# Optimization experiments

Measured on AMD Instinct MI355X. Metric: run time of the kernel, lower is better.

Reference implementation:

```python
import jax, jax.numpy as jnp
import numpy as np

B, NA, DIN, H, DOUT = 8192, 32, 8, 64, 8  # B must be divisible by NA (final reshape)


def setup_inputs() -> dict:
    key = jax.random.key(0)
    ks = jax.random.split(key, 9)
    rn = lambda k, shp, s=1.0: jax.random.normal(k, shp, dtype=jnp.float32) * s
    return {
        "x": rn(ks[0], (B, NA, DIN)),
        "laplacian": jax.random.uniform(ks[1], (B, NA, 1), dtype=jnp.float32),
        "W_in": rn(ks[2], (H, DIN), 1.0 / np.sqrt(DIN)),
        "b_in": rn(ks[3], (H,), 0.01),
        "Aq": rn(ks[4], (H, H)),   # torch.randn init in original
        "Ak": rn(ks[5], (H, H)),
        "Av": rn(ks[6], (H, H)),
        "W_out": rn(ks[7], (DOUT, H), 1.0 / np.sqrt(H)),
        "b_out": rn(ks[8], (DOUT,), 0.01),
    }


def reference(x, laplacian, W_in, b_in, Aq, Ak, Av, W_out, b_out):
    silu = jax.nn.silu
    # mlp_in = SiLU(Linear); kron(laplacian, ones(1,1,H)) == broadcast of (B,na,1) mask
    h = silu(x @ W_in.T + b_in) * laplacian            # (B, na, H)
    # Q/K/V: weight @ h^T with swish; attention is over the HIDDEN axis (H x H scores)
    Q = silu(jnp.einsum('ij,bnj->bin', Aq, h))         # (B, H, na)
    K = silu(jnp.einsum('ij,bnj->bni', Ak, h))         # (B, na, H)
    V = silu(jnp.einsum('ij,bnj->bin', Av, h))         # (B, H, na)
    A = jax.nn.softmax(jnp.einsum('bin,bnj->bij', Q, K), axis=2)  # (B, H, H), softmax dim=2
    attn = silu(jnp.einsum('bij,bjn->bni', A, V))      # (B, na, H)
    # mlp_out = SiLU(Linear), masked again, mean over nodes, reshape (B/na, na, O)
    y = silu(attn @ W_out.T + b_out) * laplacian       # (B, na, O)
    return y.mean(axis=1).reshape(-1, NA, DOUT)        # (B/NA, NA, O)
```

## Files before the change

kernel.cpp:

```cpp
#include <hip/hip_runtime.h>

#define NB   8192
#define NA   32
#define DIN  8
#define HID  64
#define DOUT 8

typedef float     v4f __attribute__((ext_vector_type(4)));
typedef __fp16    v2fp __attribute__((ext_vector_type(2)));
typedef _Float16  v2h __attribute__((ext_vector_type(2)));
typedef _Float16  v4h __attribute__((ext_vector_type(4)));
typedef _Float16  v8h __attribute__((ext_vector_type(8)));

__device__ __forceinline__ float silu_f(float x) {
    return __fdividef(x, 1.0f + __expf(-x));
}

__device__ __forceinline__ v2h pkrtz(float a, float b) {
    v2fp r = __builtin_amdgcn_cvt_pkrtz(a, b);
    return __builtin_bit_cast(v2h, r);
}

__device__ __forceinline__ v4h cvt4(v4f a) {
    v2h lo = pkrtz(a[0], a[1]);
    v2h hi = pkrtz(a[2], a[3]);
    return __builtin_shufflevector(lo, hi, 0, 1, 2, 3);
}

__device__ __forceinline__ v8h cvt8(v4f a, v4f b) {
    v4h x = cvt4(a);
    v4h y = cvt4(b);
    return __builtin_shufflevector(x, y, 0, 1, 2, 3, 4, 5, 6, 7);
}

__device__ __forceinline__ v4h silu_cvt4(v4f a) {
    v4f s;
    s[0] = silu_f(a[0]); s[1] = silu_f(a[1]);
    s[2] = silu_f(a[2]); s[3] = silu_f(a[3]);
    return cvt4(s);
}

__device__ __forceinline__ v8h cat(v4h a, v4h b) {
    return __builtin_shufflevector(a, b, 0, 1, 2, 3, 4, 5, 6, 7);
}

#define MFMA16(A, B, C) __builtin_amdgcn_mfma_f32_16x16x16f16((A), (B), (C), 0, 0, 0)
#define MFMA32(A, B, C) __builtin_amdgcn_mfma_f32_16x16x32_f16((A), (B), (C), 0, 0, 0)
#define STAGE_FENCE()   __builtin_amdgcn_sched_barrier(0)

__global__ __launch_bounds__(512, 4) void attn_mfma_kernel(
    const float* __restrict__ x,
    const float* __restrict__ lap,
    const float* __restrict__ W_in,
    const float* __restrict__ b_in,
    const float* __restrict__ Aq,
    const float* __restrict__ Ak,
    const float* __restrict__ Av,
    const float* __restrict__ W_out,
    const float* __restrict__ b_out,
    float* __restrict__ out)
{
    __shared__ _Float16 wlds[3][8][64][8];

    const int t  = threadIdx.x;
    const int l  = t & 63;
    const int w  = t >> 6;
    const int lm = l & 15;
    const int lg = l >> 4;

    {
        const float* mats[3] = {Aq, Ak, Av};
        const int it = w >> 1, c = w & 1;
        #pragma unroll
        for (int m = 0; m < 3; ++m) {
            const float* base = mats[m] + (lm + 16 * it) * 64 + 32 * c + 4 * lg;
            v4f va = *(const v4f*)(base);
            v4f vb = *(const v4f*)(base + 16);
            *(v8h*)&wlds[m][w][l][0] = cvt8(va, vb);
        }
    }

    v4h zh = {};
    v4f zf = {};
    v4h winf[4];
    #pragma unroll
    for (int jt = 0; jt < 4; ++jt) {
        v4h wf = zh;
        if (lg < 2)       wf = cvt4(*(const v4f*)(W_in + (lm + 16 * jt) * 8 + 4 * lg));
        else if (lg == 2) wf[0] = (_Float16)b_in[lm + 16 * jt];
        winf[jt] = wf;
    }
    v4h woutf[4];
    #pragma unroll
    for (int ks = 0; ks < 4; ++ks)
        woutf[ks] = (lm < 8) ? cvt4(*(const v4f*)(W_out + lm * 64 + 16 * ks + 4 * lg)) : zh;
    const float boutf = (lm < 8) ? b_out[lm] : 0.0f;
    v4h onef = zh;
    if (lg == 2) onef[0] = (_Float16)1.0f;

    __syncthreads();

    const int b = blockIdx.x * 8 + w;

    v4f lapv[2];
    lapv[0] = *(const v4f*)(lap + b * 32 + 4 * lg);
    lapv[1] = *(const v4f*)(lap + b * 32 + 16 + 4 * lg);
    float lap_n[2];
    lap_n[0] = lap[b * 32 + lm];
    lap_n[1] = lap[b * 32 + 16 + lm];

    v4h xf[2];
    #pragma unroll
    for (int nt = 0; nt < 2; ++nt)
        xf[nt] = (lg < 2) ? cvt4(*(const v4f*)(x + b * 256 + (lm + 16 * nt) * 8 + 4 * lg))
                          : onef;

    v8h hf8[2][2];
    #pragma unroll
    for (int nt = 0; nt < 2; ++nt)
        #pragma unroll
        for (int c = 0; c < 2; ++c) {
            v4h lo, hi;
            {
                v4f hc = MFMA16(winf[2 * c], xf[nt], zf);
                v4f s;
                #pragma unroll
                for (int r = 0; r < 4; ++r) s[r] = silu_f(hc[r]) * lap_n[nt];
                lo = cvt4(s);
            }
            {
                v4f hc = MFMA16(winf[2 * c + 1], xf[nt], zf);
                v4f s;
                #pragma unroll
                for (int r = 0; r < 4; ++r) s[r] = silu_f(hc[r]) * lap_n[nt];
                hi = cvt4(s);
            }
            hf8[nt][c] = cat(lo, hi);
        }
    STAGE_FENCE();

    v8h qf8[4];
    {
        v4f acc[2][4] = {};
        #pragma unroll
        for (int it = 0; it < 4; ++it)
            #pragma unroll
            for (int c = 0; c < 2; ++c) {
                v8h bw = *(v8h*)&wlds[0][it * 2 + c][l][0];
                #pragma unroll
                for (int nt = 0; nt < 2; ++nt)
                    acc[nt][it] = MFMA32(hf8[nt][c], bw, acc[nt][it]);
            }
        #pragma unroll
        for (int it = 0; it < 4; ++it)
            qf8[it] = cat(silu_cvt4(acc[0][it]), silu_cvt4(acc[1][it]));
    }
    STAGE_FENCE();

    v8h kf8[4];
    {
        v4f acc[2][4] = {};
        #pragma unroll
        for (int it = 0; it < 4; ++it)
            #pragma unroll
            for (int c = 0; c < 2; ++c) {
                v8h bw = *(v8h*)&wlds[1][it * 2 + c][l][0];
                #pragma unroll
                for (int nt = 0; nt < 2; ++nt)
                    acc[nt][it] = MFMA32(hf8[nt][c], bw, acc[nt][it]);
            }
        #pragma unroll
        for (int it = 0; it < 4; ++it)
            kf8[it] = cat(silu_cvt4(acc[0][it]), silu_cvt4(acc[1][it]));
    }
    STAGE_FENCE();

    v8h vf8[2][2];
    {
        v4f acc[4][2] = {};
        #pragma unroll
        for (int it = 0; it < 4; ++it)
            #pragma unroll
            for (int c = 0; c < 2; ++c) {
                v8h aw = *(v8h*)&wlds[2][it * 2 + c][l][0];
                #pragma unroll
                for (int nt = 0; nt < 2; ++nt)
                    acc[it][nt] = MFMA32(aw, hf8[nt][c], acc[it][nt]);
            }
        #pragma unroll
        for (int c = 0; c < 2; ++c)
            #pragma unroll
            for (int nt = 0; nt < 2; ++nt)
                vf8[c][nt] = cat(silu_cvt4(acc[2 * c][nt]), silu_cvt4(acc[2 * c + 1][nt]));
    }
    STAGE_FENCE();

    v4f ya[2] = {};
    #pragma unroll
    for (int it = 0; it < 4; ++it) {
        v4f s[4];
        #pragma unroll
        for (int jt = 0; jt < 4; ++jt)
            s[jt] = MFMA32(kf8[jt], qf8[it], zf);

        float mx = fmaxf(fmaxf(fmaxf(s[0][0], s[0][1]), fmaxf(s[0][2], s[0][3])),
                         fmaxf(fmaxf(s[1][0], s[1][1]), fmaxf(s[1][2], s[1][3])));
        float mx2 = fmaxf(fmaxf(fmaxf(s[2][0], s[2][1]), fmaxf(s[2][2], s[2][3])),
                          fmaxf(fmaxf(s[3][0], s[3][1]), fmaxf(s[3][2], s[3][3])));
        mx = fmaxf(mx, mx2);
        mx = fmaxf(mx, __shfl_xor(mx, 16, 64));
        mx = fmaxf(mx, __shfl_xor(mx, 32, 64));
        float sum = 0.0f;
        #pragma unroll
        for (int jt = 0; jt < 4; ++jt)
            #pragma unroll
            for (int r = 0; r < 4; ++r) {
                float e = __expf(s[jt][r] - mx);
                s[jt][r] = e;
                sum += e;
            }
        sum += __shfl_xor(sum, 16, 64);
        sum += __shfl_xor(sum, 32, 64);
        const float inv = __fdividef(1.0f, sum);
        v4h pf[4];
        #pragma unroll
        for (int jt = 0; jt < 4; ++jt) pf[jt] = cvt4(s[jt] * inv);

        v4f pv[2] = {};
        #pragma unroll
        for (int c = 0; c < 2; ++c) {
            v8h pf8 = cat(pf[2 * c], pf[2 * c + 1]);
            #pragma unroll
            for (int nt = 0; nt < 2; ++nt)
                pv[nt] = MFMA32(pf8, vf8[c][nt], pv[nt]);
        }

        #pragma unroll
        for (int nt = 0; nt < 2; ++nt)
            ya[nt] = MFMA16(silu_cvt4(pv[nt]), woutf[it], ya[nt]);
    }

    float acc = 0.0f;
    #pragma unroll
    for (int nt = 0; nt < 2; ++nt)
        #pragma unroll
        for (int r = 0; r < 4; ++r)
            acc += silu_f(ya[nt][r] + boutf) * lapv[nt][r];
    acc += __shfl_xor(acc, 16, 64);
    acc += __shfl_xor(acc, 32, 64);
    if (l < 8) out[b * DOUT + l] = acc * (1.0f / NA);
}

extern "C" void kernel_launch(void* const* d_in, const int* in_sizes, int n_in,
                              void* d_out, int out_size, void* d_ws, size_t ws_size,
                              hipStream_t stream) {
    const float* x     = (const float*)d_in[0];
    const float* lap   = (const float*)d_in[1];
    const float* W_in  = (const float*)d_in[2];
    const float* b_in  = (const float*)d_in[3];
    const float* Aq    = (const float*)d_in[4];
    const float* Ak    = (const float*)d_in[5];
    const float* Av    = (const float*)d_in[6];
    const float* W_out = (const float*)d_in[7];
    const float* b_out = (const float*)d_in[8];
    attn_mfma_kernel<<<1024, 512, 0, stream>>>(x, lap, W_in, b_in, Aq, Ak, Av,
                                               W_out, b_out, (float*)d_out);
}
```

Baseline: 58.79 us.

## Process two batch items per wavefront with 256-thread blocks

Each wavefront now handles two batch elements instead of one, so the block shrinks to 4 waves (256 threads) while still covering 8 items per block. Each LDS weight fragment is loaded once and reused across both items, and the two independent items give the scheduler more MFMA work to interleave. The sched_barrier stage fences are removed so the compiler can reorder freely. In exchange, register pressure roughly doubles per wave, which may lower occupancy or cause spills, and launch bounds move to (256,2).

```diff
diff --git a/kernel.cpp b/kernel.cpp
--- a/kernel.cpp
+++ b/kernel.cpp
@@ -44,11 +44,19 @@
     return __builtin_shufflevector(a, b, 0, 1, 2, 3, 4, 5, 6, 7);
 }
 
+__device__ __forceinline__ float redmax64(float x) {
+    x = fmaxf(x, __shfl_xor(x, 16, 64));
+    return fmaxf(x, __shfl_xor(x, 32, 64));
+}
+__device__ __forceinline__ float redsum64(float x) {
+    x += __shfl_xor(x, 16, 64);
+    return x + __shfl_xor(x, 32, 64);
+}
+
 #define MFMA16(A, B, C) __builtin_amdgcn_mfma_f32_16x16x16f16((A), (B), (C), 0, 0, 0)
 #define MFMA32(A, B, C) __builtin_amdgcn_mfma_f32_16x16x32_f16((A), (B), (C), 0, 0, 0)
-#define STAGE_FENCE()   __builtin_amdgcn_sched_barrier(0)
-
-__global__ __launch_bounds__(512, 4) void attn_mfma_kernel(
+
+__global__ __launch_bounds__(256, 2) void attn_mfma_kernel(
     const float* __restrict__ x,
     const float* __restrict__ lap,
     const float* __restrict__ W_in,
@@ -70,14 +78,15 @@
 
     {
         const float* mats[3] = {Aq, Ak, Av};
-        const int it = w >> 1, c = w & 1;
-        #pragma unroll
-        for (int m = 0; m < 3; ++m) {
-            const float* base = mats[m] + (lm + 16 * it) * 64 + 32 * c + 4 * lg;
-            v4f va = *(const v4f*)(base);
-            v4f vb = *(const v4f*)(base + 16);
-            *(v8h*)&wlds[m][w][l][0] = cvt8(va, vb);
-        }
+        #pragma unroll
+        for (int m = 0; m < 3; ++m)
+            #pragma unroll
+            for (int f = 0; f < 2; ++f) {
+                const int fid = w * 2 + f;
+                const float* base = mats[m] + (lm + 16 * w) * 64 + 32 * f + 4 * lg;
+                *(v8h*)&wlds[m][fid][l][0] =
+                    cvt8(*(const v4f*)base, *(const v4f*)(base + 16));
+            }
     }
 
     v4h zh = {};
@@ -100,155 +109,155 @@
 
     __syncthreads();
 
-    const int b = blockIdx.x * 8 + w;
-
-    v4f lapv[2];
-    lapv[0] = *(const v4f*)(lap + b * 32 + 4 * lg);
-    lapv[1] = *(const v4f*)(lap + b * 32 + 16 + 4 * lg);
-    float lap_n[2];
-    lap_n[0] = lap[b * 32 + lm];
-    lap_n[1] = lap[b * 32 + 16 + lm];
-
-    v4h xf[2];
-    #pragma unroll
-    for (int nt = 0; nt < 2; ++nt)
-        xf[nt] = (lg < 2) ? cvt4(*(const v4f*)(x + b * 256 + (lm + 16 * nt) * 8 + 4 * lg))
-                          : onef;
-
-    v8h hf8[2][2];
-    #pragma unroll
-    for (int nt = 0; nt < 2; ++nt)
+    const int b0 = blockIdx.x * 8 + w * 2;
+
+    v4f  lapv[2][2];
+    float lap_n[2][2];
+    v4h  xf_[2][2];
+    #pragma unroll
+    for (int u = 0; u < 2; ++u) {
+        const int b = b0 + u;
+        lapv[u][0] = *(const v4f*)(lap + b * 32 + 4 * lg);
+        lapv[u][1] = *(const v4f*)(lap + b * 32 + 16 + 4 * lg);
+        lap_n[u][0] = lap[b * 32 + lm];
+        lap_n[u][1] = lap[b * 32 + 16 + lm];
+        #pragma unroll
+        for (int nt = 0; nt < 2; ++nt)
+            xf_[u][nt] = (lg < 2)
+                ? cvt4(*(const v4f*)(x + b * 256 + (lm + 16 * nt) * 8 + 4 * lg))
+                : onef;
+    }
+
+    v8h hf8[2][2][2];
+    #pragma unroll
+    for (int u = 0; u < 2; ++u)
+        #pragma unroll
+        for (int nt = 0; nt < 2; ++nt)
+            #pragma unroll
+            for (int c = 0; c < 2; ++c) {
+                v4f h0 = MFMA16(winf[2 * c],     xf_[u][nt], zf);
+                v4f h1 = MFMA16(winf[2 * c + 1], xf_[u][nt], zf);
+                v4f s0, s1;
+                #pragma unroll
+                for (int r = 0; r < 4; ++r) {
+                    s0[r] = silu_f(h0[r]) * lap_n[u][nt];
+                    s1[r] = silu_f(h1[r]) * lap_n[u][nt];
+                }
+                hf8[u][nt][c] = cat(cvt4(s0), cvt4(s1));
+            }
+
+    v8h qf8[2][4];
+    #pragma unroll
+    for (int it = 0; it < 4; ++it) {
+        v4f a_[2][2] = {};
         #pragma unroll
         for (int c = 0; c < 2; ++c) {
-            v4h lo, hi;
-            {
-                v4f hc = MFMA16(winf[2 * c], xf[nt], zf);
-                v4f s;
-                #pragma unroll
-                for (int r = 0; r < 4; ++r) s[r] = silu_f(hc[r]) * lap_n[nt];
-                lo = cvt4(s);
-            }
-            {
-                v4f hc = MFMA16(winf[2 * c + 1], xf[nt], zf);
-                v4f s;
-                #pragma unroll
-                for (int r = 0; r < 4; ++r) s[r] = silu_f(hc[r]) * lap_n[nt];
-                hi = cvt4(s);
-            }
-            hf8[nt][c] = cat(lo, hi);
-        }
-    STAGE_FENCE();
-
-    v8h qf8[4];
-    {
-        v4f acc[2][4] = {};
-        #pragma unroll
-        for (int it = 0; it < 4; ++it)
-            #pragma unroll
-            for (int c = 0; c < 2; ++c) {
-                v8h bw = *(v8h*)&wlds[0][it * 2 + c][l][0];
+            v8h bw = *(v8h*)&wlds[0][it * 2 + c][l][0];
+            #pragma unroll
+            for (int u = 0; u < 2; ++u)
                 #pragma unroll
                 for (int nt = 0; nt < 2; ++nt)
-                    acc[nt][it] = MFMA32(hf8[nt][c], bw, acc[nt][it]);
-            }
-        #pragma unroll
-        for (int it = 0; it < 4; ++it)
-            qf8[it] = cat(silu_cvt4(acc[0][it]), silu_cvt4(acc[1][it]));
-    }
-    STAGE_FENCE();
-
-    v8h kf8[4];
-    {
-        v4f acc[2][4] = {};
-        #pragma unroll
-        for (int it = 0; it < 4; ++it)
-            #pragma unroll
-            for (int c = 0; c < 2; ++c) {
-                v8h bw = *(v8h*)&wlds[1][it * 2 + c][l][0];
+                    a_[u][nt] = MFMA32(hf8[u][nt][c], bw, a_[u][nt]);
+        }
+        #pragma unroll
+        for (int u = 0; u < 2; ++u)
+            qf8[u][it] = cat(silu_cvt4(a_[u][0]), silu_cvt4(a_[u][1]));
+    }
+    v8h kf8[2][4];
+    #pragma unroll
+    for (int it = 0; it < 4; ++it) {
+        v4f a_[2][2] = {};
+        #pragma unroll
+        for (int c = 0; c < 2; ++c) {
+            v8h bw = *(v8h*)&wlds[1][it * 2 + c][l][0];
+            #pragma unroll
+            for (int u = 0; u < 2; ++u)
                 #pragma unroll
                 for (int nt = 0; nt < 2; ++nt)
-                    acc[nt][it] = MFMA32(hf8[nt][c], bw, acc[nt][it]);
-            }
-        #pragma unroll
-        for (int it = 0; it < 4; ++it)
-            kf8[it] = cat(silu_cvt4(acc[0][it]), silu_cvt4(acc[1][it]));
-    }
-    STAGE_FENCE();
-
-    v8h vf8[2][2];
-    {
-        v4f acc[4][2] = {};
-        #pragma unroll
-        for (int it = 0; it < 4; ++it)
+                    a_[u][nt] = MFMA32(hf8[u][nt][c], bw, a_[u][nt]);
+        }
+        #pragma unroll
+        for (int u = 0; u < 2; ++u)
+            kf8[u][it] = cat(silu_cvt4(a_[u][0]), silu_cvt4(a_[u][1]));
+    }
+    v8h vf8[2][2][2];
+    #pragma unroll
+    for (int cp = 0; cp < 2; ++cp) {
+        v4f a_[2][2][2] = {};
+        #pragma unroll
+        for (int its = 0; its < 2; ++its) {
+            const int it = cp * 2 + its;
             #pragma unroll
             for (int c = 0; c < 2; ++c) {
                 v8h aw = *(v8h*)&wlds[2][it * 2 + c][l][0];
                 #pragma unroll
+                for (int u = 0; u < 2; ++u)
+                    #pragma unroll
+                    for (int nt = 0; nt < 2; ++nt)
+                        a_[its][u][nt] = MFMA32(aw, hf8[u][nt][c], a_[its][u][nt]);
+            }
+        }
+        #pragma unroll
+        for (int u = 0; u < 2; ++u)
+            #pragma unroll
+            for (int nt = 0; nt < 2; ++nt)
+                vf8[u][cp][nt] = cat(silu_cvt4(a_[0][u][nt]), silu_cvt4(a_[1][u][nt]));
+    }
+
+    v4f ya[2][2] = {};
+    #pragma unroll
+    for (int it = 0; it < 4; ++it)
+        #pragma unroll
+        for (int u = 0; u < 2; ++u) {
+            v4f s[4];
+            #pragma unroll
+            for (int jt = 0; jt < 4; ++jt)
+                s[jt] = MFMA32(kf8[u][jt], qf8[u][it], zf);
+
+            float mx = fmaxf(fmaxf(fmaxf(s[0][0], s[0][1]), fmaxf(s[0][2], s[0][3])),
+                             fmaxf(fmaxf(s[1][0], s[1][1]), fmaxf(s[1][2], s[1][3])));
+            float mx2 = fmaxf(fmaxf(fmaxf(s[2][0], s[2][1]), fmaxf(s[2][2], s[2][3])),
+                              fmaxf(fmaxf(s[3][0], s[3][1]), fmaxf(s[3][2], s[3][3])));
+            mx = redmax64(fmaxf(mx, mx2));
+            float sum = 0.0f;
+            #pragma unroll
+            for (int jt = 0; jt < 4; ++jt)
+                #pragma unroll
+                for (int r = 0; r < 4; ++r) {
+                    float e = __expf(s[jt][r] - mx);
+                    s[jt][r] = e;
+                    sum += e;
+                }
+            sum = redsum64(sum);
+            const float inv = __fdividef(1.0f, sum);
+            v4h pf[4];
+            #pragma unroll
+            for (int jt = 0; jt < 4; ++jt) pf[jt] = cvt4(s[jt] * inv);
+
+            v4f pv[2] = {};
+            #pragma unroll
+            for (int c = 0; c < 2; ++c) {
+                v8h pf8 = cat(pf[2 * c], pf[2 * c + 1]);
+                #pragma unroll
                 for (int nt = 0; nt < 2; ++nt)
-                    acc[it][nt] = MFMA32(aw, hf8[nt][c], acc[it][nt]);
-            }
-        #pragma unroll
-        for (int c = 0; c < 2; ++c)
+                    pv[nt] = MFMA32(pf8, vf8[u][c][nt], pv[nt]);
+            }
             #pragma unroll
             for (int nt = 0; nt < 2; ++nt)
-                vf8[c][nt] = cat(silu_cvt4(acc[2 * c][nt]), silu_cvt4(acc[2 * c + 1][nt]));
-    }
-    STAGE_FENCE();
-
-    v4f ya[2] = {};
-    #pragma unroll
-    for (int it = 0; it < 4; ++it) {
-        v4f s[4];
-        #pragma unroll
-        for (int jt = 0; jt < 4; ++jt)
-            s[jt] = MFMA32(kf8[jt], qf8[it], zf);
-
-        float mx = fmaxf(fmaxf(fmaxf(s[0][0], s[0][1]), fmaxf(s[0][2], s[0][3])),
-                         fmaxf(fmaxf(s[1][0], s[1][1]), fmaxf(s[1][2], s[1][3])));
-        float mx2 = fmaxf(fmaxf(fmaxf(s[2][0], s[2][1]), fmaxf(s[2][2], s[2][3])),
-                          fmaxf(fmaxf(s[3][0], s[3][1]), fmaxf(s[3][2], s[3][3])));
-        mx = fmaxf(mx, mx2);
-        mx = fmaxf(mx, __shfl_xor(mx, 16, 64));
-        mx = fmaxf(mx, __shfl_xor(mx, 32, 64));
-        float sum = 0.0f;
-        #pragma unroll
-        for (int jt = 0; jt < 4; ++jt)
-            #pragma unroll
-            for (int r = 0; r < 4; ++r) {
-                float e = __expf(s[jt][r] - mx);
-                s[jt][r] = e;
-                sum += e;
-            }
-        sum += __shfl_xor(sum, 16, 64);
-        sum += __shfl_xor(sum, 32, 64);
-        const float inv = __fdividef(1.0f, sum);
-        v4h pf[4];
-        #pragma unroll
-        for (int jt = 0; jt < 4; ++jt) pf[jt] = cvt4(s[jt] * inv);
-
-        v4f pv[2] = {};
-        #pragma unroll
-        for (int c = 0; c < 2; ++c) {
-            v8h pf8 = cat(pf[2 * c], pf[2 * c + 1]);
-            #pragma unroll
-            for (int nt = 0; nt < 2; ++nt)
-                pv[nt] = MFMA32(pf8, vf8[c][nt], pv[nt]);
-        }
-
+                ya[u][nt] = MFMA16(silu_cvt4(pv[nt]), woutf[it], ya[u][nt]);
+        }
+
+    #pragma unroll
+    for (int u = 0; u < 2; ++u) {
+        float acc = 0.0f;
         #pragma unroll
         for (int nt = 0; nt < 2; ++nt)
-            ya[nt] = MFMA16(silu_cvt4(pv[nt]), woutf[it], ya[nt]);
-    }
-
-    float acc = 0.0f;
-    #pragma unroll
-    for (int nt = 0; nt < 2; ++nt)
-        #pragma unroll
-        for (int r = 0; r < 4; ++r)
-            acc += silu_f(ya[nt][r] + boutf) * lapv[nt][r];
-    acc += __shfl_xor(acc, 16, 64);
-    acc += __shfl_xor(acc, 32, 64);
-    if (l < 8) out[b * DOUT + l] = acc * (1.0f / NA);
+            #pragma unroll
+            for (int r = 0; r < 4; ++r)
+                acc += silu_f(ya[u][nt][r] + boutf) * lapv[u][nt][r];
+        acc = redsum64(acc);
+        if (l < 8) out[(b0 + u) * DOUT + l] = acc * (1.0f / NA);
+    }
 }
 
 extern "C" void kernel_launch(void* const* d_in, const int* in_sizes, int n_in,
@@ -263,6 +272,6 @@
     const float* Av    = (const float*)d_in[6];
     const float* W_out = (const float*)d_in[7];
     const float* b_out = (const float*)d_in[8];
-    attn_mfma_kernel<<<1024, 512, 0, stream>>>(x, lap, W_in, b_in, Aq, Ak, Av,
+    attn_mfma_kernel<<<1024, 256, 0, stream>>>(x, lap, W_in, b_in, Aq, Ak, Av,
                                                W_out, b_out, (float*)d_out);
 }
```

Measured after the change: 57.68 us. About the same (-1.9%).

## Halve block size, drop stage sched barriers, defer W_out and lap loads

Applied to the files above, without the earlier changes.

Moves from 512-thread blocks of 8 batches to 256-thread blocks of 4 batches, so each wave now stages two weight fragments per matrix into LDS. Removes the sched_barrier fences between stages, which lets the compiler interleave MFMAs and SiLU across stages. Moves the W_out, b_out and laplacian-vector loads to just before the attention loop to shorten their live ranges and ease register pressure. The trade-off is that LDS weight staging is now amortized over fewer batches per block, and the schedule is left entirely to the compiler.

```diff
diff --git a/kernel.cpp b/kernel.cpp
--- a/kernel.cpp
+++ b/kernel.cpp
@@ -44,11 +44,19 @@
     return __builtin_shufflevector(a, b, 0, 1, 2, 3, 4, 5, 6, 7);
 }
 
+__device__ __forceinline__ float redmax64(float x) {
+    x = fmaxf(x, __shfl_xor(x, 16, 64));
+    return fmaxf(x, __shfl_xor(x, 32, 64));
+}
+__device__ __forceinline__ float redsum64(float x) {
+    x += __shfl_xor(x, 16, 64);
+    return x + __shfl_xor(x, 32, 64);
+}
+
 #define MFMA16(A, B, C) __builtin_amdgcn_mfma_f32_16x16x16f16((A), (B), (C), 0, 0, 0)
 #define MFMA32(A, B, C) __builtin_amdgcn_mfma_f32_16x16x32_f16((A), (B), (C), 0, 0, 0)
-#define STAGE_FENCE()   __builtin_amdgcn_sched_barrier(0)
-
-__global__ __launch_bounds__(512, 4) void attn_mfma_kernel(
+
+__global__ __launch_bounds__(256, 4) void attn_mfma_kernel(
     const float* __restrict__ x,
     const float* __restrict__ lap,
     const float* __restrict__ W_in,
@@ -70,14 +78,15 @@
 
     {
         const float* mats[3] = {Aq, Ak, Av};
-        const int it = w >> 1, c = w & 1;
-        #pragma unroll
-        for (int m = 0; m < 3; ++m) {
-            const float* base = mats[m] + (lm + 16 * it) * 64 + 32 * c + 4 * lg;
-            v4f va = *(const v4f*)(base);
-            v4f vb = *(const v4f*)(base + 16);
-            *(v8h*)&wlds[m][w][l][0] = cvt8(va, vb);
-        }
+        #pragma unroll
+        for (int m = 0; m < 3; ++m)
+            #pragma unroll
+            for (int f = 0; f < 2; ++f) {
+                const int fid = w * 2 + f;
+                const float* base = mats[m] + (lm + 16 * w) * 64 + 32 * f + 4 * lg;
+                *(v8h*)&wlds[m][fid][l][0] =
+                    cvt8(*(const v4f*)base, *(const v4f*)(base + 16));
+            }
     }
 
     v4h zh = {};
@@ -90,21 +99,13 @@
         else if (lg == 2) wf[0] = (_Float16)b_in[lm + 16 * jt];
         winf[jt] = wf;
     }
-    v4h woutf[4];
-    #pragma unroll
-    for (int ks = 0; ks < 4; ++ks)
-        woutf[ks] = (lm < 8) ? cvt4(*(const v4f*)(W_out + lm * 64 + 16 * ks + 4 * lg)) : zh;
-    const float boutf = (lm < 8) ? b_out[lm] : 0.0f;
     v4h onef = zh;
     if (lg == 2) onef[0] = (_Float16)1.0f;
 
     __syncthreads();
 
-    const int b = blockIdx.x * 8 + w;
-
-    v4f lapv[2];
-    lapv[0] = *(const v4f*)(lap + b * 32 + 4 * lg);
-    lapv[1] = *(const v4f*)(lap + b * 32 + 16 + 4 * lg);
+    const int b = blockIdx.x * 4 + w;
+
     float lap_n[2];
     lap_n[0] = lap[b * 32 + lm];
     lap_n[1] = lap[b * 32 + 16 + lm];
@@ -120,24 +121,16 @@
     for (int nt = 0; nt < 2; ++nt)
         #pragma unroll
         for (int c = 0; c < 2; ++c) {
-            v4h lo, hi;
-            {
-                v4f hc = MFMA16(winf[2 * c], xf[nt], zf);
-                v4f s;
-                #pragma unroll
-                for (int r = 0; r < 4; ++r) s[r] = silu_f(hc[r]) * lap_n[nt];
-                lo = cvt4(s);
-            }
-            {
-                v4f hc = MFMA16(winf[2 * c + 1], xf[nt], zf);
-                v4f s;
-                #pragma unroll
-                for (int r = 0; r < 4; ++r) s[r] = silu_f(hc[r]) * lap_n[nt];
-                hi = cvt4(s);
-            }
-            hf8[nt][c] = cat(lo, hi);
+            v4f h0 = MFMA16(winf[2 * c],     xf[nt], zf);
+            v4f h1 = MFMA16(winf[2 * c + 1], xf[nt], zf);
+            v4f s0, s1;
+            #pragma unroll
+            for (int r = 0; r < 4; ++r) {
+                s0[r] = silu_f(h0[r]) * lap_n[nt];
+                s1[r] = silu_f(h1[r]) * lap_n[nt];
+            }
+            hf8[nt][c] = cat(cvt4(s0), cvt4(s1));
         }
-    STAGE_FENCE();
 
     v8h qf8[4];
     {
@@ -155,8 +148,6 @@
         for (int it = 0; it < 4; ++it)
             qf8[it] = cat(silu_cvt4(acc[0][it]), silu_cvt4(acc[1][it]));
     }
-    STAGE_FENCE();
-
     v8h kf8[4];
     {
         v4f acc[2][4] = {};
@@ -173,8 +164,6 @@
         for (int it = 0; it < 4; ++it)
             kf8[it] = cat(silu_cvt4(acc[0][it]), silu_cvt4(acc[1][it]));
     }
-    STAGE_FENCE();
-
     v8h vf8[2][2];
     {
         v4f acc[4][2] = {};
@@ -193,7 +182,15 @@
             for (int nt = 0; nt < 2; ++nt)
                 vf8[c][nt] = cat(silu_cvt4(acc[2 * c][nt]), silu_cvt4(acc[2 * c + 1][nt]));
     }
-    STAGE_FENCE();
+
+    v4h woutf[4];
+    #pragma unroll
+    for (int ks = 0; ks < 4; ++ks)
+        woutf[ks] = (lm < 8) ? cvt4(*(const v4f*)(W_out + lm * 64 + 16 * ks + 4 * lg)) : zh;
+    const float boutf = (lm < 8) ? b_out[lm] : 0.0f;
+    v4f lapv[2];
+    lapv[0] = *(const v4f*)(lap + b * 32 + 4 * lg);
+    lapv[1] = *(const v4f*)(lap + b * 32 + 16 + 4 * lg);
 
     v4f ya[2] = {};
     #pragma unroll
@@ -207,9 +204,7 @@
                          fmaxf(fmaxf(s[1][0], s[1][1]), fmaxf(s[1][2], s[1][3])));
         float mx2 = fmaxf(fmaxf(fmaxf(s[2][0], s[2][1]), fmaxf(s[2][2], s[2][3])),
                           fmaxf(fmaxf(s[3][0], s[3][1]), fmaxf(s[3][2], s[3][3])));
-        mx = fmaxf(mx, mx2);
-        mx = fmaxf(mx, __shfl_xor(mx, 16, 64));
-        mx = fmaxf(mx, __shfl_xor(mx, 32, 64));
+        mx = redmax64(fmaxf(mx, mx2));
         float sum = 0.0f;
         #pragma unroll
         for (int jt = 0; jt < 4; ++jt)
@@ -219,8 +214,7 @@
                 s[jt][r] = e;
                 sum += e;
             }
-        sum += __shfl_xor(sum, 16, 64);
-        sum += __shfl_xor(sum, 32, 64);
+        sum = redsum64(sum);
         const float inv = __fdividef(1.0f, sum);
         v4h pf[4];
         #pragma unroll
@@ -234,7 +228,6 @@
             for (int nt = 0; nt < 2; ++nt)
                 pv[nt] = MFMA32(pf8, vf8[c][nt], pv[nt]);
         }
-
         #pragma unroll
         for (int nt = 0; nt < 2; ++nt)
             ya[nt] = MFMA16(silu_cvt4(pv[nt]), woutf[it], ya[nt]);
@@ -246,8 +239,7 @@
         #pragma unroll
         for (int r = 0; r < 4; ++r)
             acc += silu_f(ya[nt][r] + boutf) * lapv[nt][r];
-    acc += __shfl_xor(acc, 16, 64);
-    acc += __shfl_xor(acc, 32, 64);
+    acc = redsum64(acc);
     if (l < 8) out[b * DOUT + l] = acc * (1.0f / NA);
 }
 
@@ -263,6 +255,6 @@
     const float* Av    = (const float*)d_in[6];
     const float* W_out = (const float*)d_in[7];
     const float* b_out = (const float*)d_in[8];
-    attn_mfma_kernel<<<1024, 512, 0, stream>>>(x, lap, W_in, b_in, Aq, Ak, Av,
+    attn_mfma_kernel<<<2048, 256, 0, stream>>>(x, lap, W_in, b_in, Aq, Ak, Av,
                                                W_out, b_out, (float*)d_out);
 }
```

Result: faster. 56.53 us, median of 3 (-3.8%).
